# Performance work log

Hardware: AMD Instinct MI355X
Metric: run time of the kernel (lower is better)

## Reference

```python
import math
import jax, jax.numpy as jnp
import numpy as np

D_MODEL = 1024
N_HEADS = 16
D_K = D_MODEL // N_HEADS


def setup_inputs() -> dict:
    key = jax.random.key(0)
    ks = jax.random.split(key, 12)
    B, L, D = 8, 2048, D_MODEL
    scale = 1.0 / math.sqrt(D)
    inp = {
        "queries": jax.random.normal(ks[0], (B, L, D), jnp.float32),
        "keys": jax.random.normal(ks[1], (B, L, D), jnp.float32),
        "values": jax.random.normal(ks[2], (B, L, D), jnp.float32),
        "Wq": jax.random.normal(ks[3], (D, D), jnp.float32) * scale,
        "bq": jnp.zeros((D,), jnp.float32),
        "Wk": jax.random.normal(ks[4], (D, D), jnp.float32) * scale,
        "bk": jnp.zeros((D,), jnp.float32),
        "Wv": jax.random.normal(ks[5], (D, D), jnp.float32) * scale,
        "bv": jnp.zeros((D,), jnp.float32),
        "Wo": jax.random.normal(ks[6], (D, D), jnp.float32) * scale,
        "bo": jnp.zeros((D,), jnp.float32),
    }
    return inp


def _autocorr_forward(queries, keys, values, Wq, bq, Wk, bk, Wv, bv, Wo, bo):
    B, L, D = queries.shape
    H, dk = N_HEADS, D_K
    # projections (torch Linear: x @ W.T + b), split heads -> [B, L, H, dk]
    q = (queries @ Wq.T + bq).reshape(B, L, H, dk)
    k = (keys @ Wk.T + bk).reshape(B, L, H, dk)
    v = (values @ Wv.T + bv).reshape(B, L, H, dk)

    # FFT cross-correlation along time, averaged over channel dim: [B, L, H]
    qf = jnp.fft.rfft(q, axis=1)
    kf = jnp.fft.rfft(k, axis=1)
    corr = jnp.fft.irfft(qf * jnp.conj(kf), n=L, axis=1).mean(axis=-1)
    corr = corr.transpose(0, 2, 1)  # [B, H, L]

    topk = min(max(1, int(math.log(L))), L)  # top_k=None default
    weights, delays = jax.lax.top_k(corr, topk)  # [B, H, k]
    w = jax.nn.softmax(weights, axis=-1)

    # modulo-shifted gather indices: [B, H, k, L]
    idx = (jnp.arange(L)[None, None, None, :] - delays[..., None]) % L
    v_h = v.transpose(0, 2, 1, 3)  # [B, H, L, dk]
    # gather shifted copies: [B, H, k, L, dk]
    gathered = jnp.take_along_axis(v_h[:, :, None], idx[..., None], axis=3)
    out = (w[..., None, None] * gathered).sum(axis=2)  # [B, H, L, dk]

    out = out.transpose(0, 2, 1, 3).reshape(B, L, D)
    return out @ Wo.T + bo


def reference(queries, keys, values, Wq, bq, Wk, bk, Wv, bv, Wo, bo):
    return _autocorr_forward(queries, keys, values, Wq, bq, Wk, bk, Wv, bv, Wo, bo)
```

## Files before the change

kernel.cpp:

```cpp
#include <hip/hip_runtime.h>
#include <hip/hip_bf16.h>
#include <math.h>

#define B_SZ 8
#define L_SZ 2048
#define D_SZ 1024
#define H_SZ 16
#define DK_SZ 64
#define TOPK 7
#define M_SZ (B_SZ * L_SZ)

typedef __attribute__((ext_vector_type(8))) short short8;
typedef __attribute__((ext_vector_type(4))) float float4v;
typedef unsigned short ushort_t;
typedef unsigned int uint_t;

__device__ __forceinline__ ushort_t f2bf(float x) {
    uint_t u = __float_as_uint(x);
    uint_t r = (u + 0x7fffu + ((u >> 16) & 1u)) >> 16;
    return (ushort_t)r;
}

__device__ __forceinline__ void split8(float4 x, float4 y, short8& hi, short8& lo) {
    float f[8] = {x.x, x.y, x.z, x.w, y.x, y.y, y.z, y.w};
#pragma unroll
    for (int i = 0; i < 8; ++i) {
        uint_t b = __float_as_uint(f[i]);
        hi[i] = (short)(b >> 16);
        float r = f[i] - __uint_as_float(b & 0xffff0000u);
        lo[i] = (short)(__float_as_uint(r) >> 16);
    }
}

__device__ __forceinline__ void gl_lds16(const ushort_t* g, ushort_t* l) {
    __builtin_amdgcn_global_load_lds(
        (const __attribute__((address_space(1))) unsigned int*)g,
        (__attribute__((address_space(3))) unsigned int*)l, 16, 0, 0);
}

__global__ __launch_bounds__(256)
void zero_f32(float* __restrict__ p, int n4) {
    int i = blockIdx.x * 256 + threadIdx.x;
    if (i < n4) ((float4*)p)[i] = make_float4(0.f, 0.f, 0.f, 0.f);
}

__global__ __launch_bounds__(256)
void split_fp32(const float* __restrict__ X, ushort_t* __restrict__ hi,
                ushort_t* __restrict__ lo, int n8) {
    int i = blockIdx.x * 256 + threadIdx.x;
    if (i >= n8) return;
    float4 a = ((const float4*)X)[2 * i];
    float4 b = ((const float4*)X)[2 * i + 1];
    short8 h, l;
    split8(a, b, h, l);
    *(short8*)(hi + (size_t)i * 8) = h;
    *(short8*)(lo + (size_t)i * 8) = l;
}

__global__ __launch_bounds__(256)
void split_fp32_x4(const float* __restrict__ W0, const float* __restrict__ W1,
                   const float* __restrict__ W2, const float* __restrict__ W3,
                   ushort_t* __restrict__ dst) {
    const int w = blockIdx.y;
    const float* X = (w == 0) ? W0 : (w == 1) ? W1 : (w == 2) ? W2 : W3;
    ushort_t* hi = dst + (size_t)w * 2097152;
    ushort_t* lo = hi + 1048576;
    const int i = blockIdx.x * 256 + threadIdx.x;
    float4 a = ((const float4*)X)[2 * i];
    float4 b = ((const float4*)X)[2 * i + 1];
    short8 h, l;
    split8(a, b, h, l);
    *(short8*)(hi + (size_t)i * 8) = h;
    *(short8*)(lo + (size_t)i * 8) = l;
}

template <bool BF16OUT>
__global__ __launch_bounds__(256)
void gemm_split_mfma(const float* __restrict__ X, const ushort_t* __restrict__ Whi,
                     const ushort_t* __restrict__ Wlo, const float* __restrict__ bias,
                     void* __restrict__ Yv, int M, int N, int K) {
    __shared__ __align__(16) short Ah[4][128][8];
    __shared__ __align__(16) short Al[4][128][8];
    __shared__ __align__(16) short Bh[4][128][8];
    __shared__ __align__(16) short Bl[4][128][8];

    const int tid = threadIdx.x;
    const int lane = tid & 63;
    const int wave = tid >> 6;
    const int wm = wave >> 1, wn = wave & 1;

    const int flat = blockIdx.y * gridDim.x + blockIdx.x;
    const int cpx  = (gridDim.x * gridDim.y) >> 3;
    const int swz  = (flat & 7) * cpx + (flat >> 3);
    const int bx   = swz % gridDim.x;
    const int by   = swz / gridDim.x;
    const size_t m0 = (size_t)by * 128;
    const size_t n0 = (size_t)bx * 128;

    const int srow = tid >> 1;
    const int g0 = (tid & 1) * 2;
    const int skseg = (tid & 1) * 16;

    const float*    Xp  = X   + (m0 + srow) * K + skseg;
    const ushort_t* Whp = Whi + (n0 + srow) * K + skseg;
    const ushort_t* Wlp = Wlo + (n0 + srow) * K + skseg;

    const int fr = lane & 15;
    const int fg = lane >> 4;

    float4 ax0 = *(const float4*)(Xp + 0);
    float4 ax1 = *(const float4*)(Xp + 4);
    float4 ax2 = *(const float4*)(Xp + 8);
    float4 ax3 = *(const float4*)(Xp + 12);
    short8 bh0 = *(const short8*)(Whp + 0);
    short8 bh1 = *(const short8*)(Whp + 8);
    short8 bl0 = *(const short8*)(Wlp + 0);
    short8 bl1 = *(const short8*)(Wlp + 8);

    float4v acc[4][4];
#pragma unroll
    for (int i = 0; i < 4; ++i)
#pragma unroll
        for (int j = 0; j < 4; ++j) acc[i][j] = (float4v){0.f, 0.f, 0.f, 0.f};

    for (int k0 = 0; k0 < K; k0 += 32) {
        __syncthreads();
        short8 h, l;
        split8(ax0, ax1, h, l);
        *(short8*)&Ah[g0][srow][0] = h;      *(short8*)&Al[g0][srow][0] = l;
        split8(ax2, ax3, h, l);
        *(short8*)&Ah[g0 + 1][srow][0] = h;  *(short8*)&Al[g0 + 1][srow][0] = l;
        *(short8*)&Bh[g0][srow][0] = bh0;    *(short8*)&Bh[g0 + 1][srow][0] = bh1;
        *(short8*)&Bl[g0][srow][0] = bl0;    *(short8*)&Bl[g0 + 1][srow][0] = bl1;
        __syncthreads();

        if (k0 + 32 < K) {
            ax0 = *(const float4*)(Xp + k0 + 32);
            ax1 = *(const float4*)(Xp + k0 + 36);
            ax2 = *(const float4*)(Xp + k0 + 40);
            ax3 = *(const float4*)(Xp + k0 + 44);
            bh0 = *(const short8*)(Whp + k0 + 32);
            bh1 = *(const short8*)(Whp + k0 + 40);
            bl0 = *(const short8*)(Wlp + k0 + 32);
            bl1 = *(const short8*)(Wlp + k0 + 40);
        }

        short8 afh[4], afl[4], bfh[4], bfl[4];
#pragma unroll
        for (int i = 0; i < 4; ++i) {
            const int r = wm * 64 + i * 16 + fr;
            afh[i] = *(const short8*)&Ah[fg][r][0];
            afl[i] = *(const short8*)&Al[fg][r][0];
        }
#pragma unroll
        for (int j = 0; j < 4; ++j) {
            const int r = wn * 64 + j * 16 + fr;
            bfh[j] = *(const short8*)&Bh[fg][r][0];
            bfl[j] = *(const short8*)&Bl[fg][r][0];
        }
#pragma unroll
        for (int i = 0; i < 4; ++i)
#pragma unroll
            for (int j = 0; j < 4; ++j) {
                acc[i][j] = __builtin_amdgcn_mfma_f32_16x16x32_bf16(afh[i], bfh[j], acc[i][j], 0, 0, 0);
                acc[i][j] = __builtin_amdgcn_mfma_f32_16x16x32_bf16(afh[i], bfl[j], acc[i][j], 0, 0, 0);
                acc[i][j] = __builtin_amdgcn_mfma_f32_16x16x32_bf16(afl[i], bfh[j], acc[i][j], 0, 0, 0);
            }
    }

    const int en = fr;
    const int emb = (lane >> 4) * 4;
#pragma unroll
    for (int j = 0; j < 4; ++j) {
        const size_t col = n0 + wn * 64 + j * 16 + en;
        const float bv = bias[col];
#pragma unroll
        for (int i = 0; i < 4; ++i) {
#pragma unroll
            for (int r = 0; r < 4; ++r) {
                const size_t row = m0 + wm * 64 + i * 16 + emb + r;
                const float o = acc[i][j][r] + bv;
                if (BF16OUT) ((ushort_t*)Yv)[row * N + col] = f2bf(o);
                else         ((float*)Yv)[row * N + col] = o;
            }
        }
    }
}

__global__ __launch_bounds__(256)
void corr_mfma(const ushort_t* __restrict__ Qb, const ushort_t* __restrict__ Kb,
               float* __restrict__ corr) {
    __shared__ __align__(16) ushort_t Qlds[28 * 1024];
    __shared__ __align__(16) ushort_t Klds[4 * 1024];

    const int tid  = threadIdx.x;
    const int wave = tid >> 6;
    const int lane = tid & 63;
    const int bh = blockIdx.x;
    const int jq = blockIdx.y;
    const int b = bh >> 4, h = bh & 15;
    const int b0 = jq * 32;
    const int jbase = b0 + wave * 8;
    const int rr = lane & 15;
    const int cq = lane >> 4;
    const int s7 = rr & 7;

    const size_t slice = (size_t)b * L_SZ * D_SZ + (size_t)h * DK_SZ;
    const ushort_t* Qs = Qb + slice;
    const ushort_t* Ks = Kb + slice;
    const ushort_t* Qp = Qs + cq * 8;

    const int st  = tid & 127;
    const int sr  = st >> 3;
    const int sc  = (st & 7) ^ (sr & 7);
    const int whalf = (wave & 1) * 512;

    const int roff0 = rr * 64 + ((cq ^ s7) * 8);
    const int roff1 = roff0 ^ 32;

    float4v acc[8];
#pragma unroll
    for (int i = 0; i < 8; ++i) acc[i] = (float4v){0.f, 0.f, 0.f, 0.f};

    if (wave < 2) {
        for (int i = 0; i < 26; ++i) {
            const int qt = (b0 + 8 + i) & 127;
            gl_lds16(Qs + (size_t)(qt * 16 + sr) * 1024 + sc * 8,
                     &Qlds[i * 1024 + whalf]);
        }
    } else {
        for (int i = 0; i < 3; ++i) {
            gl_lds16(Ks + (size_t)(i * 16 + sr) * 1024 + sc * 8,
                     &Klds[i * 1024 + whalf]);
        }
    }

    short8 Wa[8], Wb[8];
#pragma unroll
    for (int i = 0; i < 8; ++i) {
        const size_t tq = (size_t)((((jbase + i) & 127) << 4) + rr) * D_SZ;
        Wa[i] = *(const short8*)(Qp + tq);
        Wb[i] = *(const short8*)(Qp + tq + 32);
    }

    asm volatile("s_waitcnt vmcnt(0)" ::: "memory");
    __builtin_amdgcn_s_barrier();
    asm volatile("" ::: "memory");

    short8 kb0 = *(const short8*)&Klds[roff0];
    short8 kb1 = *(const short8*)&Klds[roff1];

    int qsr = wave * 8;
    int qsw = 26;

    for (int s8 = 0; s8 < 128; s8 += 8) {
#pragma unroll
        for (int u = 0; u < 8; ++u) {
            const int s0 = s8 + u;
            if (wave < 2) {
                const int qt = (b0 + 34 + s0) & 127;
                gl_lds16(Qs + (size_t)(qt * 16 + sr) * 1024 + sc * 8,
                         &Qlds[qsw * 1024 + whalf]);
            } else {
                const int kt = (s0 + 3) & 127;
                gl_lds16(Ks + (size_t)(kt * 16 + sr) * 1024 + sc * 8,
                         &Klds[((s0 + 3) & 3) * 1024 + whalf]);
            }
            asm volatile("s_waitcnt vmcnt(2)" ::: "memory");
            __builtin_amdgcn_s_barrier();
            asm volatile("" ::: "memory");

            const int kslot = ((s0 + 1) & 3) * 1024;
            short8 nk0 = *(const short8*)&Klds[kslot + roff0];
            short8 nk1 = *(const short8*)&Klds[kslot + roff1];

            acc[0] = __builtin_amdgcn_mfma_f32_16x16x32_bf16(Wa[u], kb0, acc[0], 0, 0, 0);
            acc[0] = __builtin_amdgcn_mfma_f32_16x16x32_bf16(Wb[u], kb1, acc[0], 0, 0, 0);
            {
                const int qbse = qsr * 1024;
                Wa[u] = *(const short8*)&Qlds[qbse + roff0];
                Wb[u] = *(const short8*)&Qlds[qbse + roff1];
            }
#pragma unroll
            for (int jj = 1; jj < 8; ++jj) {
                acc[jj] = __builtin_amdgcn_mfma_f32_16x16x32_bf16(Wa[(u + jj) & 7], kb0, acc[jj], 0, 0, 0);
                acc[jj] = __builtin_amdgcn_mfma_f32_16x16x32_bf16(Wb[(u + jj) & 7], kb1, acc[jj], 0, 0, 0);
            }
            kb0 = nk0; kb1 = nk1;
            qsr = (qsr + 1 == 28) ? 0 : qsr + 1;
            qsw = (qsw + 1 == 28) ? 0 : qsw + 1;
        }
    }

    const int n = lane & 15;
    const int mb = (lane >> 4) * 4;
    float* cb = corr + (size_t)bh * L_SZ;
#pragma unroll
    for (int jj = 0; jj < 8; ++jj) {
        const int j16 = (jbase + jj) << 4;
#pragma unroll
        for (int r = 0; r < 4; ++r) {
            const int d = (j16 + mb + r - n) & (L_SZ - 1);
            atomicAdd(cb + d, acc[jj][r] * (1.0f / 64.0f));
        }
    }
}

__global__ __launch_bounds__(256)
void topk_softmax(const float* __restrict__ corr, float* __restrict__ w,
                  int* __restrict__ delays) {
    __shared__ float cv[L_SZ];
    __shared__ float wvv[4];
    __shared__ int   wvi[4];
    __shared__ float topv[TOPK];
    __shared__ int   topi[TOPK];
    const int bh = blockIdx.x, tid = threadIdx.x;
    const int lane = tid & 63, wid = tid >> 6;

    for (int i = tid; i < L_SZ; i += 256) cv[i] = corr[(size_t)bh * L_SZ + i];
    __syncthreads();

    for (int it = 0; it < TOPK; ++it) {
        float best = -INFINITY; int bi = 0;
        for (int i = tid; i < L_SZ; i += 256) {
            float x = cv[i];
            if (x > best) { best = x; bi = i; }
        }
#pragma unroll
        for (int off = 32; off > 0; off >>= 1) {
            float ov = __shfl_down(best, off);
            int   oi = __shfl_down(bi, off);
            if (ov > best || (ov == best && oi < bi)) { best = ov; bi = oi; }
        }
        if (lane == 0) { wvv[wid] = best; wvi[wid] = bi; }
        __syncthreads();
        if (tid == 0) {
            float bb = wvv[0]; int bbi = wvi[0];
#pragma unroll
            for (int k = 1; k < 4; ++k)
                if (wvv[k] > bb || (wvv[k] == bb && wvi[k] < bbi)) { bb = wvv[k]; bbi = wvi[k]; }
            topv[it] = bb; topi[it] = bbi;
            cv[bbi] = -INFINITY;
        }
        __syncthreads();
    }

    if (tid == 0) {
        float mx = topv[0];
        float e[TOPK], s = 0.f;
#pragma unroll
        for (int i = 0; i < TOPK; ++i) { e[i] = expf(topv[i] - mx); s += e[i]; }
        const float inv = 1.0f / s;
#pragma unroll
        for (int i = 0; i < TOPK; ++i) {
            w[bh * TOPK + i] = e[i] * inv;
            delays[bh * TOPK + i] = topi[i];
        }
    }
}

__global__ __launch_bounds__(256)
void gather_combine(const float* __restrict__ V, const float* __restrict__ w,
                    const int* __restrict__ delays, float* __restrict__ mid) {
    const size_t g = (size_t)blockIdx.x * 256 + threadIdx.x;
    const int c4 = (int)(g & 255);
    const int t  = (int)((g >> 8) & (L_SZ - 1));
    const int b  = (int)(g >> 19);
    const int h  = c4 >> 4;
    const int bh = b * H_SZ + h;
    const size_t colbase = (size_t)b * L_SZ * D_SZ + (size_t)c4 * 4;

    float4 acc = {0.f, 0.f, 0.f, 0.f};
#pragma unroll
    for (int i = 0; i < TOPK; ++i) {
        const float wi = w[bh * TOPK + i];
        const int   di = delays[bh * TOPK + i];
        const int   ts = (t - di) & (L_SZ - 1);
        float4 v4 = *(const float4*)(V + colbase + (size_t)ts * D_SZ);
        acc.x += wi * v4.x; acc.y += wi * v4.y;
        acc.z += wi * v4.z; acc.w += wi * v4.w;
    }
    *(float4*)(mid + (size_t)b * L_SZ * D_SZ + (size_t)t * D_SZ + c4 * 4) = acc;
}

extern "C" void kernel_launch(void* const* d_in, const int* in_sizes, int n_in,
                              void* d_out, int out_size, void* d_ws, size_t ws_size,
                              hipStream_t stream) {
    const float* queries = (const float*)d_in[0];
    const float* keys    = (const float*)d_in[1];
    const float* values  = (const float*)d_in[2];
    const float* Wq = (const float*)d_in[3];
    const float* bq = (const float*)d_in[4];
    const float* Wk = (const float*)d_in[5];
    const float* bk = (const float*)d_in[6];
    const float* Wv = (const float*)d_in[7];
    const float* bv = (const float*)d_in[8];
    const float* Wo = (const float*)d_in[9];
    const float* bo = (const float*)d_in[10];

    const size_t NE = (size_t)M_SZ * D_SZ;
    const size_t WNE = (size_t)D_SZ * D_SZ;
    ushort_t* Qb16 = (ushort_t*)d_ws;
    ushort_t* Kb16 = Qb16 + NE;
    float* Vb   = (float*)(Kb16 + NE);
    float* corr = Vb + NE;
    float* wbuf = corr + (size_t)B_SZ * H_SZ * L_SZ;
    int*   dbuf = (int*)(wbuf + B_SZ * H_SZ * TOPK);
    ushort_t* WS = (ushort_t*)(dbuf + B_SZ * H_SZ * TOPK);
    float* mid  = (float*)d_ws;

    dim3 ggemm(D_SZ / 128, M_SZ / 128);
    const int wn8 = (int)(WNE / 8);

    const size_t ws_off  = (size_t)((char*)WS - (char*)d_ws);
    const bool batched = ws_size >= ws_off + 4 * 2 * WNE * sizeof(ushort_t);

    if (batched) {
        split_fp32_x4<<<dim3(512, 4), 256, 0, stream>>>(Wq, Wk, Wv, Wo, WS);
        gemm_split_mfma<true><<<ggemm, 256, 0, stream>>>(
            queries, WS + 0 * 2 * WNE, WS + 0 * 2 * WNE + WNE, bq, Qb16, M_SZ, D_SZ, D_SZ);
        gemm_split_mfma<true><<<ggemm, 256, 0, stream>>>(
            keys,    WS + 1 * 2 * WNE, WS + 1 * 2 * WNE + WNE, bk, Kb16, M_SZ, D_SZ, D_SZ);
        gemm_split_mfma<false><<<ggemm, 256, 0, stream>>>(
            values,  WS + 2 * 2 * WNE, WS + 2 * 2 * WNE + WNE, bv, Vb, M_SZ, D_SZ, D_SZ);
    } else {
        ushort_t* WH = WS;
        ushort_t* WL = WS + WNE;
        split_fp32<<<(wn8 + 255) / 256, 256, 0, stream>>>(Wq, WH, WL, wn8);
        gemm_split_mfma<true><<<ggemm, 256, 0, stream>>>(queries, WH, WL, bq, Qb16, M_SZ, D_SZ, D_SZ);
        split_fp32<<<(wn8 + 255) / 256, 256, 0, stream>>>(Wk, WH, WL, wn8);
        gemm_split_mfma<true><<<ggemm, 256, 0, stream>>>(keys, WH, WL, bk, Kb16, M_SZ, D_SZ, D_SZ);
        split_fp32<<<(wn8 + 255) / 256, 256, 0, stream>>>(Wv, WH, WL, wn8);
        gemm_split_mfma<false><<<ggemm, 256, 0, stream>>>(values, WH, WL, bv, Vb, M_SZ, D_SZ, D_SZ);
    }

    zero_f32<<<(B_SZ * H_SZ * L_SZ / 4 + 255) / 256, 256, 0, stream>>>(
        corr, B_SZ * H_SZ * L_SZ / 4);

    corr_mfma<<<dim3(B_SZ * H_SZ, 4), 256, 0, stream>>>(Qb16, Kb16, corr);

    topk_softmax<<<B_SZ * H_SZ, 256, 0, stream>>>(corr, wbuf, dbuf);

    gather_combine<<<(M_SZ * 256) / 256, 256, 0, stream>>>(Vb, wbuf, dbuf, mid);

    if (batched) {
        gemm_split_mfma<false><<<ggemm, 256, 0, stream>>>(
            mid, WS + 3 * 2 * WNE, WS + 3 * 2 * WNE + WNE, bo, (float*)d_out, M_SZ, D_SZ, D_SZ);
    } else {
        ushort_t* WH = WS;
        ushort_t* WL = WS + WNE;
        split_fp32<<<(wn8 + 255) / 256, 256, 0, stream>>>(Wo, WH, WL, wn8);
        gemm_split_mfma<false><<<ggemm, 256, 0, stream>>>(mid, WH, WL, bo, (float*)d_out, M_SZ, D_SZ, D_SZ);
    }
}
```

Baseline: 785.9 us.

## Replace split-bf16 GEMM with 256x256 double-buffered, swizzled LDS kernel

Swaps the 128x128 split-precision GEMM for a 512-thread kernel with 256x256 tiles and 8 waves. It double-buffers LDS, loads the weight tiles directly into LDS through gl_lds16, and XOR-swizzles the LDS layout to avoid bank conflicts. The three MFMA passes (hi*hi, hi*lo, lo*hi) are staged with s_setprio and barriers. The aim is more reuse per tile and hiding global latency behind compute in the four projection GEMMs that dominate runtime. The costs are higher register and LDS pressure, and M, N and K are now hard-coded to the problem sizes.

```diff
diff --git a/kernel.cpp b/kernel.cpp
--- a/kernel.cpp
+++ b/kernel.cpp
@@ -75,113 +75,157 @@
 }
 
 template <bool BF16OUT>
-__global__ __launch_bounds__(256)
-void gemm_split_mfma(const float* __restrict__ X, const ushort_t* __restrict__ Whi,
-                     const ushort_t* __restrict__ Wlo, const float* __restrict__ bias,
-                     void* __restrict__ Yv, int M, int N, int K) {
-    __shared__ __align__(16) short Ah[4][128][8];
-    __shared__ __align__(16) short Al[4][128][8];
-    __shared__ __align__(16) short Bh[4][128][8];
-    __shared__ __align__(16) short Bl[4][128][8];
+__global__ __launch_bounds__(512, 2)
+void gemm256(const float* __restrict__ X, const ushort_t* __restrict__ Whi,
+             const ushort_t* __restrict__ Wlo, const float* __restrict__ bias,
+             void* __restrict__ Yv) {
+    __shared__ __align__(16) ushort_t Ab[2][256][64];
+    __shared__ __align__(16) ushort_t Bb[2][256][64];
 
     const int tid = threadIdx.x;
     const int lane = tid & 63;
     const int wave = tid >> 6;
-    const int wm = wave >> 1, wn = wave & 1;
-
-    const int flat = blockIdx.y * gridDim.x + blockIdx.x;
-    const int cpx  = (gridDim.x * gridDim.y) >> 3;
-    const int swz  = (flat & 7) * cpx + (flat >> 3);
-    const int bx   = swz % gridDim.x;
-    const int by   = swz / gridDim.x;
-    const size_t m0 = (size_t)by * 128;
-    const size_t n0 = (size_t)bx * 128;
-
-    const int srow = tid >> 1;
-    const int g0 = (tid & 1) * 2;
-    const int skseg = (tid & 1) * 16;
-
-    const float*    Xp  = X   + (m0 + srow) * K + skseg;
-    const ushort_t* Whp = Whi + (n0 + srow) * K + skseg;
-    const ushort_t* Wlp = Wlo + (n0 + srow) * K + skseg;
+    const int wm = wave >> 2;
+    const int wn = wave & 3;
+
+    const int flat = blockIdx.y * 4 + blockIdx.x;
+    const int swz  = (flat & 7) * 32 + (flat >> 3);
+    const size_t n0 = (size_t)(swz & 3) * 256;
+    const size_t m0 = (size_t)(swz >> 2) * 256;
+
+    const int arow = tid >> 1;
+    const int ah   = tid & 1;
+    const float* Xp = X + (m0 + arow) * D_SZ + ah * 16;
+    const int rswA = (arow & 7) ^ (((arow >> 3) & 1) << 2);
+    const int sh0 = (2 * ah) ^ rswA;
+    const int sh1 = (2 * ah + 1) ^ rswA;
+    ushort_t* Awr = &Ab[0][arow][0];
+
+    const ushort_t* bsrc[4];
+    int bdst[4];
+#pragma unroll
+    for (int i = 0; i < 4; ++i) {
+        const int G   = i * 512 + tid;
+        const int row = G >> 3;
+        const int slt = G & 7;
+        const int g   = slt ^ (row & 7) ^ (((row >> 3) & 1) << 2);
+        bsrc[i] = ((g < 4) ? Whi : Wlo) + (n0 + row) * D_SZ + (g & 3) * 8;
+        bdst[i] = G * 8;
+    }
 
     const int fr = lane & 15;
     const int fg = lane >> 4;
+    int offA[8], offB[4];
+#pragma unroll
+    for (int f = 0; f < 8; ++f) {
+        const int r = wm * 128 + f * 16 + fr;
+        offA[f] = r * 64 + (fg ^ ((r & 7) ^ (((r >> 3) & 1) << 2))) * 8;
+    }
+#pragma unroll
+    for (int j = 0; j < 4; ++j) {
+        const int r = wn * 64 + j * 16 + fr;
+        offB[j] = r * 64 + (fg ^ ((r & 7) ^ (((r >> 3) & 1) << 2))) * 8;
+    }
+
+    float4v acc[8][4];
+#pragma unroll
+    for (int f = 0; f < 8; ++f)
+#pragma unroll
+        for (int j = 0; j < 4; ++j) acc[f][j] = (float4v){0.f, 0.f, 0.f, 0.f};
 
     float4 ax0 = *(const float4*)(Xp + 0);
     float4 ax1 = *(const float4*)(Xp + 4);
     float4 ax2 = *(const float4*)(Xp + 8);
     float4 ax3 = *(const float4*)(Xp + 12);
-    short8 bh0 = *(const short8*)(Whp + 0);
-    short8 bh1 = *(const short8*)(Whp + 8);
-    short8 bl0 = *(const short8*)(Wlp + 0);
-    short8 bl1 = *(const short8*)(Wlp + 8);
-
-    float4v acc[4][4];
-#pragma unroll
-    for (int i = 0; i < 4; ++i)
-#pragma unroll
-        for (int j = 0; j < 4; ++j) acc[i][j] = (float4v){0.f, 0.f, 0.f, 0.f};
-
-    for (int k0 = 0; k0 < K; k0 += 32) {
-        __syncthreads();
+#pragma unroll
+    for (int i = 0; i < 4; ++i) gl_lds16(bsrc[i], &Bb[0][0][0] + bdst[i]);
+    {
         short8 h, l;
         split8(ax0, ax1, h, l);
-        *(short8*)&Ah[g0][srow][0] = h;      *(short8*)&Al[g0][srow][0] = l;
+        *(short8*)(Awr + sh0 * 8) = h;  *(short8*)(Awr + (sh0 ^ 4) * 8) = l;
         split8(ax2, ax3, h, l);
-        *(short8*)&Ah[g0 + 1][srow][0] = h;  *(short8*)&Al[g0 + 1][srow][0] = l;
-        *(short8*)&Bh[g0][srow][0] = bh0;    *(short8*)&Bh[g0 + 1][srow][0] = bh1;
-        *(short8*)&Bl[g0][srow][0] = bl0;    *(short8*)&Bl[g0 + 1][srow][0] = bl1;
+        *(short8*)(Awr + sh1 * 8) = h;  *(short8*)(Awr + (sh1 ^ 4) * 8) = l;
+    }
+    __syncthreads();
+
+    for (int t = 0; t < 32; ++t) {
+        const int cur = t & 1;
+        const ushort_t* Ac = &Ab[cur][0][0];
+        const ushort_t* Bc = &Bb[cur][0][0];
+        const bool pf = (t + 1 < 32);
+
+        if (pf) {
+            const int kn = (t + 1) * 32;
+            ax0 = *(const float4*)(Xp + kn + 0);
+            ax1 = *(const float4*)(Xp + kn + 4);
+            ax2 = *(const float4*)(Xp + kn + 8);
+            ax3 = *(const float4*)(Xp + kn + 12);
+            ushort_t* Bn = &Bb[cur ^ 1][0][0];
+#pragma unroll
+            for (int i = 0; i < 4; ++i) gl_lds16(bsrc[i] + kn, Bn + bdst[i]);
+        }
+
+        short8 fAh[8], fBh[4];
+#pragma unroll
+        for (int f = 0; f < 8; ++f) fAh[f] = *(const short8*)(Ac + offA[f]);
+#pragma unroll
+        for (int j = 0; j < 4; ++j) fBh[j] = *(const short8*)(Bc + offB[j]);
+        __builtin_amdgcn_s_setprio(1);
+#pragma unroll
+        for (int f = 0; f < 8; ++f)
+#pragma unroll
+            for (int j = 0; j < 4; ++j)
+                acc[f][j] = __builtin_amdgcn_mfma_f32_16x16x32_bf16(fAh[f], fBh[j], acc[f][j], 0, 0, 0);
+        __builtin_amdgcn_s_setprio(0);
+        __builtin_amdgcn_s_barrier();
+
+        short8 fBl[4];
+#pragma unroll
+        for (int j = 0; j < 4; ++j) fBl[j] = *(const short8*)(Bc + (offB[j] ^ 32));
+        __builtin_amdgcn_s_setprio(1);
+#pragma unroll
+        for (int f = 0; f < 8; ++f)
+#pragma unroll
+            for (int j = 0; j < 4; ++j)
+                acc[f][j] = __builtin_amdgcn_mfma_f32_16x16x32_bf16(fAh[f], fBl[j], acc[f][j], 0, 0, 0);
+        __builtin_amdgcn_s_setprio(0);
+        __builtin_amdgcn_s_barrier();
+
+        short8 fAl[8];
+#pragma unroll
+        for (int f = 0; f < 8; ++f) fAl[f] = *(const short8*)(Ac + (offA[f] ^ 32));
+        __builtin_amdgcn_s_setprio(1);
+#pragma unroll
+        for (int f = 0; f < 8; ++f)
+#pragma unroll
+            for (int j = 0; j < 4; ++j)
+                acc[f][j] = __builtin_amdgcn_mfma_f32_16x16x32_bf16(fAl[f], fBh[j], acc[f][j], 0, 0, 0);
+        __builtin_amdgcn_s_setprio(0);
+
+        if (pf) {
+            ushort_t* Aw = Awr + (cur ^ 1) * 16384;
+            short8 h, l;
+            split8(ax0, ax1, h, l);
+            *(short8*)(Aw + sh0 * 8) = h;  *(short8*)(Aw + (sh0 ^ 4) * 8) = l;
+            split8(ax2, ax3, h, l);
+            *(short8*)(Aw + sh1 * 8) = h;  *(short8*)(Aw + (sh1 ^ 4) * 8) = l;
+        }
         __syncthreads();
-
-        if (k0 + 32 < K) {
-            ax0 = *(const float4*)(Xp + k0 + 32);
-            ax1 = *(const float4*)(Xp + k0 + 36);
-            ax2 = *(const float4*)(Xp + k0 + 40);
-            ax3 = *(const float4*)(Xp + k0 + 44);
-            bh0 = *(const short8*)(Whp + k0 + 32);
-            bh1 = *(const short8*)(Whp + k0 + 40);
-            bl0 = *(const short8*)(Wlp + k0 + 32);
-            bl1 = *(const short8*)(Wlp + k0 + 40);
-        }
-
-        short8 afh[4], afl[4], bfh[4], bfl[4];
-#pragma unroll
-        for (int i = 0; i < 4; ++i) {
-            const int r = wm * 64 + i * 16 + fr;
-            afh[i] = *(const short8*)&Ah[fg][r][0];
-            afl[i] = *(const short8*)&Al[fg][r][0];
-        }
-#pragma unroll
-        for (int j = 0; j < 4; ++j) {
-            const int r = wn * 64 + j * 16 + fr;
-            bfh[j] = *(const short8*)&Bh[fg][r][0];
-            bfl[j] = *(const short8*)&Bl[fg][r][0];
-        }
-#pragma unroll
-        for (int i = 0; i < 4; ++i)
-#pragma unroll
-            for (int j = 0; j < 4; ++j) {
-                acc[i][j] = __builtin_amdgcn_mfma_f32_16x16x32_bf16(afh[i], bfh[j], acc[i][j], 0, 0, 0);
-                acc[i][j] = __builtin_amdgcn_mfma_f32_16x16x32_bf16(afh[i], bfl[j], acc[i][j], 0, 0, 0);
-                acc[i][j] = __builtin_amdgcn_mfma_f32_16x16x32_bf16(afl[i], bfh[j], acc[i][j], 0, 0, 0);
-            }
-    }
-
-    const int en = fr;
+    }
+
     const int emb = (lane >> 4) * 4;
 #pragma unroll
     for (int j = 0; j < 4; ++j) {
-        const size_t col = n0 + wn * 64 + j * 16 + en;
+        const size_t col = n0 + wn * 64 + j * 16 + fr;
         const float bv = bias[col];
 #pragma unroll
-        for (int i = 0; i < 4; ++i) {
+        for (int f = 0; f < 8; ++f) {
 #pragma unroll
             for (int r = 0; r < 4; ++r) {
-                const size_t row = m0 + wm * 64 + i * 16 + emb + r;
-                const float o = acc[i][j][r] + bv;
-                if (BF16OUT) ((ushort_t*)Yv)[row * N + col] = f2bf(o);
-                else         ((float*)Yv)[row * N + col] = o;
+                const size_t row = m0 + wm * 128 + f * 16 + emb + r;
+                const float o = acc[f][j][r] + bv;
+                if (BF16OUT) ((ushort_t*)Yv)[row * D_SZ + col] = f2bf(o);
+                else         ((float*)Yv)[row * D_SZ + col] = o;
             }
         }
     }
@@ -409,7 +453,7 @@
     ushort_t* WS = (ushort_t*)(dbuf + B_SZ * H_SZ * TOPK);
     float* mid  = (float*)d_ws;
 
-    dim3 ggemm(D_SZ / 128, M_SZ / 128);
+    dim3 ggemm(D_SZ / 256, M_SZ / 256);
     const int wn8 = (int)(WNE / 8);
 
     const size_t ws_off  = (size_t)((char*)WS - (char*)d_ws);
@@ -417,21 +461,21 @@
 
     if (batched) {
         split_fp32_x4<<<dim3(512, 4), 256, 0, stream>>>(Wq, Wk, Wv, Wo, WS);
-        gemm_split_mfma<true><<<ggemm, 256, 0, stream>>>(
-            queries, WS + 0 * 2 * WNE, WS + 0 * 2 * WNE + WNE, bq, Qb16, M_SZ, D_SZ, D_SZ);
-        gemm_split_mfma<true><<<ggemm, 256, 0, stream>>>(
-            keys,    WS + 1 * 2 * WNE, WS + 1 * 2 * WNE + WNE, bk, Kb16, M_SZ, D_SZ, D_SZ);
-        gemm_split_mfma<false><<<ggemm, 256, 0, stream>>>(
-            values,  WS + 2 * 2 * WNE, WS + 2 * 2 * WNE + WNE, bv, Vb, M_SZ, D_SZ, D_SZ);
+        gemm256<true><<<ggemm, 512, 0, stream>>>(
+            queries, WS + 0 * 2 * WNE, WS + 0 * 2 * WNE + WNE, bq, Qb16);
+        gemm256<true><<<ggemm, 512, 0, stream>>>(
+            keys,    WS + 1 * 2 * WNE, WS + 1 * 2 * WNE + WNE, bk, Kb16);
+        gemm256<false><<<ggemm, 512, 0, stream>>>(
+            values,  WS + 2 * 2 * WNE, WS + 2 * 2 * WNE + WNE, bv, Vb);
     } else {
         ushort_t* WH = WS;
         ushort_t* WL = WS + WNE;
         split_fp32<<<(wn8 + 255) / 256, 256, 0, stream>>>(Wq, WH, WL, wn8);
-        gemm_split_mfma<true><<<ggemm, 256, 0, stream>>>(queries, WH, WL, bq, Qb16, M_SZ, D_SZ, D_SZ);
+        gemm256<true><<<ggemm, 512, 0, stream>>>(queries, WH, WL, bq, Qb16);
         split_fp32<<<(wn8 + 255) / 256, 256, 0, stream>>>(Wk, WH, WL, wn8);
-        gemm_split_mfma<true><<<ggemm, 256, 0, stream>>>(keys, WH, WL, bk, Kb16, M_SZ, D_SZ, D_SZ);
+        gemm256<true><<<ggemm, 512, 0, stream>>>(keys, WH, WL, bk, Kb16);
         split_fp32<<<(wn8 + 255) / 256, 256, 0, stream>>>(Wv, WH, WL, wn8);
-        gemm_split_mfma<false><<<ggemm, 256, 0, stream>>>(values, WH, WL, bv, Vb, M_SZ, D_SZ, D_SZ);
+        gemm256<false><<<ggemm, 512, 0, stream>>>(values, WH, WL, bv, Vb);
     }
 
     zero_f32<<<(B_SZ * H_SZ * L_SZ / 4 + 255) / 256, 256, 0, stream>>>(
@@ -444,12 +488,12 @@
     gather_combine<<<(M_SZ * 256) / 256, 256, 0, stream>>>(Vb, wbuf, dbuf, mid);
 
     if (batched) {
-        gemm_split_mfma<false><<<ggemm, 256, 0, stream>>>(
-            mid, WS + 3 * 2 * WNE, WS + 3 * 2 * WNE + WNE, bo, (float*)d_out, M_SZ, D_SZ, D_SZ);
+        gemm256<false><<<ggemm, 512, 0, stream>>>(
+            mid, WS + 3 * 2 * WNE, WS + 3 * 2 * WNE + WNE, bo, (float*)d_out);
     } else {
         ushort_t* WH = WS;
         ushort_t* WL = WS + WNE;
         split_fp32<<<(wn8 + 255) / 256, 256, 0, stream>>>(Wo, WH, WL, wn8);
-        gemm_split_mfma<false><<<ggemm, 256, 0, stream>>>(mid, WH, WL, bo, (float*)d_out, M_SZ, D_SZ, D_SZ);
-    }
-}
+        gemm256<false><<<ggemm, 512, 0, stream>>>(mid, WH, WL, bo, (float*)d_out);
+    }
+}
```

New measurement: 775.0 us. Within noise of the previous version (-1.4%).
